# Optimization experiments

Measured on AMD Instinct MI355X. Metric: run time of the kernel, lower is better.

## Reference

```python
import jax, jax.numpy as jnp
import numpy as np
import math

B, S, DM, H = 2, 2048, 1024, 16
HD = DM // H  # head_dim = 64


def setup_inputs() -> dict:
    key = jax.random.key(0)
    ks = jax.random.split(key, 7)
    mk = lambda k, shp, s=1.0: jax.random.normal(k, shp, dtype=jnp.float32) * s
    return {
        "q": mk(ks[0], (B, S, DM)),
        "k": mk(ks[1], (B, S, DM)),
        "v": mk(ks[2], (B, S, DM)),
        "wq": mk(ks[3], (DM, DM), 0.02),
        "wk": mk(ks[4], (DM, DM), 0.02),
        "wv": mk(ks[5], (DM, DM), 0.02),
        "wo": mk(ks[6], (DM, DM), 0.02),
    }


def reference(q, k, v, wq, wk, wv, wo):
    bsz, seqlen, _ = q.shape
    # bias-free linear projections: y = x @ W.T (torch nn.Linear layout [out,in])
    def proj(x, w):
        y = jnp.einsum('bsd,ed->bse', x, w)
        return y.reshape(bsz, seqlen, H, HD).transpose(0, 2, 1, 3)  # (B,H,S,HD)
    xq, xk, xv = proj(q, wq), proj(k, wk), proj(v, wv)
    scores = jnp.einsum('bhqd,bhkd->bhqk', xq, xk) / math.sqrt(HD)  # (B,H,S,S)
    # causal mask: -inf above the diagonal
    causal = jnp.tril(jnp.ones((seqlen, seqlen), dtype=bool))
    scores = jnp.where(causal[None, None], scores, -jnp.inf)
    probs = jax.nn.softmax(scores.astype(jnp.float32), axis=-1).astype(xq.dtype)
    # dropout p=0.0 -> identity in eval / p=0 config
    out = jnp.einsum('bhqk,bhkd->bhqd', probs, xv)  # (B,H,S,HD)
    out = out.transpose(0, 2, 1, 3).reshape(bsz, seqlen, DM)
    return jnp.einsum('bsd,ed->bse', out, wo)
```

## Files before the change

### kernel.cpp

```cpp
#include <hip/hip_runtime.h>
#include <hip/hip_bf16.h>
#include <stdint.h>

#define NB 2
#define NS 2048
#define NDM 1024
#define NH 16
#define NHD 64
#define NTOK (NB * NS)

typedef __bf16 bf16x8 __attribute__((ext_vector_type(8)));
typedef float f32x4 __attribute__((ext_vector_type(4)));
typedef uint16_t u16x8 __attribute__((ext_vector_type(8)));

static __device__ __forceinline__ uint16_t f2bf(float f) {
  __bf16 b = (__bf16)f;
  union { __bf16 b; uint16_t u; } x; x.b = b;
  return x.u;
}

static __device__ __forceinline__ u16x8 cvt8(float4 a, float4 b) {
  u16x8 v;
  v[0] = f2bf(a.x); v[1] = f2bf(a.y); v[2] = f2bf(a.z); v[3] = f2bf(a.w);
  v[4] = f2bf(b.x); v[5] = f2bf(b.y); v[6] = f2bf(b.z); v[7] = f2bf(b.w);
  return v;
}

static __device__ __forceinline__ void gload_lds16(const void* g, void* l) {
  __builtin_amdgcn_global_load_lds(
      (const __attribute__((address_space(1))) void*)g,
      (__attribute__((address_space(3))) void*)l, 16, 0, 0);
}

__global__ __launch_bounds__(256) void cvt_w(
    const float* __restrict__ w0, const float* __restrict__ w1,
    const float* __restrict__ w2, const float* __restrict__ w3,
    uint16_t* __restrict__ o0, uint16_t* __restrict__ o1,
    uint16_t* __restrict__ o2, uint16_t* __restrict__ o3) {
  int y = blockIdx.y;
  const float* src = (y == 0) ? w0 : (y == 1) ? w1 : (y == 2) ? w2 : w3;
  uint16_t* dst = (y == 0) ? o0 : (y == 1) ? o1 : (y == 2) ? o2 : o3;
  int i = ((int)blockIdx.x * 256 + (int)threadIdx.x) * 8;
  float4 a = *(const float4*)(src + i);
  float4 b = *(const float4*)(src + i + 4);
  *(u16x8*)&dst[i] = cvt8(a, b);
}

__global__ __launch_bounds__(256) void proj_gemm(
    const float* __restrict__ q, const float* __restrict__ k,
    const float* __restrict__ v, const uint16_t* __restrict__ wqb,
    const uint16_t* __restrict__ wkb, const uint16_t* __restrict__ wvb,
    uint16_t* __restrict__ XQ, uint16_t* __restrict__ XK,
    uint16_t* __restrict__ XVT) {
  __shared__ uint16_t As[2][128][64];
  __shared__ uint16_t Bs[2][128][64];
  int z = blockIdx.z;
  const float* A = (z == 0) ? q : (z == 1) ? k : v;
  const uint16_t* W = (z == 0) ? wqb : (z == 1) ? wkb : wvb;
  int m0 = blockIdx.x * 128, n0 = blockIdx.y * 128;
  int tid = threadIdx.x;
  int lane = tid & 63, w = tid >> 6;
  int g = lane >> 4, r16 = lane & 15;
  int wm = w >> 1, wn = w & 1;
  int bce = ((lane & 7) ^ ((lane >> 3) & 7)) * 8;
  int brlane = lane >> 3;

  f32x4 acc[4][4] = {};
  float4 a0[4], a1[4];

  #pragma unroll
  for (int cc = 0; cc < 4; ++cc) {
    int ch = tid + cc * 256;
    int row = ch >> 3, c8 = ch & 7;
    const float* src = A + (size_t)(m0 + row) * NDM + c8 * 8;
    a0[cc] = *(const float4*)src;
    a1[cc] = *(const float4*)(src + 4);
  }
  #pragma unroll
  for (int i = 0; i < 4; ++i) {
    int brow = w * 32 + i * 8;
    gload_lds16(W + (size_t)(n0 + brow + brlane) * NDM + bce, &Bs[0][brow][0]);
  }
  #pragma unroll
  for (int cc = 0; cc < 4; ++cc) {
    int ch = tid + cc * 256;
    int row = ch >> 3, c8 = ch & 7;
    *(u16x8*)&As[0][row][((c8 ^ (row & 7)) * 8)] = cvt8(a0[cc], a1[cc]);
  }
  #pragma unroll
  for (int cc = 0; cc < 4; ++cc) {
    int ch = tid + cc * 256;
    int row = ch >> 3, c8 = ch & 7;
    const float* src = A + (size_t)(m0 + row) * NDM + 64 + c8 * 8;
    a0[cc] = *(const float4*)src;
    a1[cc] = *(const float4*)(src + 4);
  }
  __syncthreads();

  for (int t = 0; t < 16; ++t) {
    int cur = t & 1, nxt = cur ^ 1;
    if (t < 15) {
      int k1 = (t + 1) * 64;
      #pragma unroll
      for (int i = 0; i < 4; ++i) {
        int brow = w * 32 + i * 8;
        gload_lds16(W + (size_t)(n0 + brow + brlane) * NDM + k1 + bce,
                    &Bs[nxt][brow][0]);
      }
      #pragma unroll
      for (int cc = 0; cc < 4; ++cc) {
        int ch = tid + cc * 256;
        int row = ch >> 3, c8 = ch & 7;
        *(u16x8*)&As[nxt][row][((c8 ^ (row & 7)) * 8)] = cvt8(a0[cc], a1[cc]);
      }
      if (t < 14) {
        int k2 = (t + 2) * 64;
        #pragma unroll
        for (int cc = 0; cc < 4; ++cc) {
          int ch = tid + cc * 256;
          int row = ch >> 3, c8 = ch & 7;
          const float* src = A + (size_t)(m0 + row) * NDM + k2 + c8 * 8;
          a0[cc] = *(const float4*)src;
          a1[cc] = *(const float4*)(src + 4);
        }
      }
    }

    #pragma unroll
    for (int kc = 0; kc < 2; ++kc) {
      bf16x8 af[4], bf[4];
      #pragma unroll
      for (int i = 0; i < 4; ++i) {
        int gran = (kc * 4 + g) ^ (r16 & 7);
        af[i] = *(const bf16x8*)&As[cur][wm * 64 + i * 16 + r16][gran * 8];
        bf[i] = *(const bf16x8*)&Bs[cur][wn * 64 + i * 16 + r16][gran * 8];
      }
      #pragma unroll
      for (int mi = 0; mi < 4; ++mi)
        #pragma unroll
        for (int ni = 0; ni < 4; ++ni)
          acc[mi][ni] = __builtin_amdgcn_mfma_f32_16x16x32_bf16(
              af[mi], bf[ni], acc[mi][ni], 0, 0, 0);
    }
    __syncthreads();
  }

  float scale = (z == 0) ? 0.125f * 1.44269504088896340736f : 1.0f;
  #pragma unroll
  for (int mi = 0; mi < 4; ++mi) {
    #pragma unroll
    for (int ni = 0; ni < 4; ++ni) {
      int m = m0 + wm * 64 + mi * 16 + g * 4;
      int n = n0 + wn * 64 + ni * 16 + r16;
      f32x4 a = acc[mi][ni];
      if (z == 2) {
        ushort4 pk;
        pk.x = f2bf(a[0]); pk.y = f2bf(a[1]);
        pk.z = f2bf(a[2]); pk.w = f2bf(a[3]);
        *(ushort4*)&XVT[(size_t)n * NTOK + m] = pk;
      } else {
        uint16_t* Y = (z == 0) ? XQ : XK;
        #pragma unroll
        for (int j = 0; j < 4; ++j)
          Y[(size_t)(m + j) * NDM + n] = f2bf(a[j] * scale);
      }
    }
  }
}

__global__ __launch_bounds__(256) void attn_kernel(
    const uint16_t* __restrict__ XQ, const uint16_t* __restrict__ XK,
    const uint16_t* __restrict__ XVT, uint16_t* __restrict__ AO) {
  __shared__ uint16_t Klds[64][72];
  __shared__ uint16_t Vlds[64][72];
  __shared__ uint16_t Plds[4][16][72];

  int tid = threadIdx.x;
  int lane = tid & 63;
  int w = tid >> 6;
  int g = lane >> 4, r16 = lane & 15;
  int srow = tid >> 2;
  int scol = (tid & 3) * 16;

  int item = (int)blockIdx.x;
  int qc = 31 - (item >> 5);
  int bh = item & 31;
  int b = bh >> 4, h = bh & 15;
  int q0 = qc * 64;
  int q0w = q0 + w * 16;
  int T = qc + 1;

  const uint16_t* qb =
      XQ + (size_t)(b * NS + q0w + r16) * NDM + h * NHD + g * 8;
  bf16x8 qf0 = *(const bf16x8*)qb;
  bf16x8 qf1 = *(const bf16x8*)(qb + 32);

  f32x4 oacc[4] = {};
  float mrow = -1e30f, lsum = 0.f;

  const uint16_t* kbase = XK + (size_t)(b * NS + srow) * NDM + h * NHD + scol;
  const uint16_t* vbase = XVT + (size_t)(h * NHD + srow) * NTOK + b * NS + scol;

  u16x8 kr0 = *(const u16x8*)(kbase);
  u16x8 kr1 = *(const u16x8*)(kbase + 8);
  u16x8 vr0 = *(const u16x8*)(vbase);
  u16x8 vr1 = *(const u16x8*)(vbase + 8);

  for (int t = 0; t < T; ++t) {
    int kv0 = t * 64;
    __syncthreads();
    *(u16x8*)&Klds[srow][scol]     = kr0;
    *(u16x8*)&Klds[srow][scol + 8] = kr1;
    *(u16x8*)&Vlds[srow][scol]     = vr0;
    *(u16x8*)&Vlds[srow][scol + 8] = vr1;
    __syncthreads();
    if (t + 1 < T) {
      const uint16_t* kp = kbase + (size_t)(t + 1) * 64 * NDM;
      const uint16_t* vp = vbase + (t + 1) * 64;
      kr0 = *(const u16x8*)(kp);
      kr1 = *(const u16x8*)(kp + 8);
      vr0 = *(const u16x8*)(vp);
      vr1 = *(const u16x8*)(vp + 8);
    }

    f32x4 sc[4];
    __builtin_amdgcn_s_setprio(1);
    #pragma unroll
    for (int t4 = 0; t4 < 4; ++t4) {
      bf16x8 kf0 = *(const bf16x8*)&Klds[t4 * 16 + r16][g * 8];
      bf16x8 kf1 = *(const bf16x8*)&Klds[t4 * 16 + r16][32 + g * 8];
      f32x4 x = __builtin_amdgcn_mfma_f32_16x16x32_bf16(
          kf0, qf0, (f32x4){0.f, 0.f, 0.f, 0.f}, 0, 0, 0);
      x = __builtin_amdgcn_mfma_f32_16x16x32_bf16(kf1, qf1, x, 0, 0, 0);
      sc[t4] = x;
    }
    __builtin_amdgcn_s_setprio(0);

    #pragma unroll
    for (int t4 = 0; t4 < 4; ++t4) {
      if (kv0 + t4 * 16 + 15 > q0w) {
        #pragma unroll
        for (int j = 0; j < 4; ++j)
          if (kv0 + t4 * 16 + g * 4 + j > q0w + r16) sc[t4][j] = -1e30f;
      }
    }

    float m16 = fmaxf(
        fmaxf(fmaxf(fmaxf(sc[0][0], sc[0][1]), fmaxf(sc[0][2], sc[0][3])),
              fmaxf(fmaxf(sc[1][0], sc[1][1]), fmaxf(sc[1][2], sc[1][3]))),
        fmaxf(fmaxf(fmaxf(sc[2][0], sc[2][1]), fmaxf(sc[2][2], sc[2][3])),
              fmaxf(fmaxf(sc[3][0], sc[3][1]), fmaxf(sc[3][2], sc[3][3]))));
    m16 = fmaxf(m16, __shfl_xor(m16, 16));
    m16 = fmaxf(m16, __shfl_xor(m16, 32));

    if (!__all(m16 <= mrow + 8.0f)) {
      float mnew = fmaxf(mrow, m16);
      float sf = __builtin_amdgcn_exp2f(mrow - mnew);
      mrow = mnew;
      lsum *= sf;
      #pragma unroll
      for (int j = 0; j < 4; ++j) {
        float sfj = __shfl(sf, g * 4 + j);
        #pragma unroll
        for (int dt = 0; dt < 4; ++dt) oacc[dt][j] *= sfj;
      }
    }

    #pragma unroll
    for (int t4 = 0; t4 < 4; ++t4) {
      float p0 = __builtin_amdgcn_exp2f(sc[t4][0] - mrow);
      float p1 = __builtin_amdgcn_exp2f(sc[t4][1] - mrow);
      float p2 = __builtin_amdgcn_exp2f(sc[t4][2] - mrow);
      float p3 = __builtin_amdgcn_exp2f(sc[t4][3] - mrow);
      lsum += (p0 + p1) + (p2 + p3);
      ushort4 pk;
      pk.x = f2bf(p0); pk.y = f2bf(p1); pk.z = f2bf(p2); pk.w = f2bf(p3);
      *(ushort4*)&Plds[w][r16][t4 * 16 + g * 4] = pk;
    }

    bf16x8 pa0 = *(const bf16x8*)&Plds[w][r16][g * 8];
    bf16x8 pa1 = *(const bf16x8*)&Plds[w][r16][32 + g * 8];
    __builtin_amdgcn_s_setprio(1);
    #pragma unroll
    for (int dt = 0; dt < 4; ++dt) {
      bf16x8 vf0 = *(const bf16x8*)&Vlds[dt * 16 + r16][g * 8];
      bf16x8 vf1 = *(const bf16x8*)&Vlds[dt * 16 + r16][32 + g * 8];
      oacc[dt] = __builtin_amdgcn_mfma_f32_16x16x32_bf16(pa0, vf0, oacc[dt], 0, 0, 0);
      oacc[dt] = __builtin_amdgcn_mfma_f32_16x16x32_bf16(pa1, vf1, oacc[dt], 0, 0, 0);
    }
    __builtin_amdgcn_s_setprio(0);
  }

  float l2 = lsum + __shfl_xor(lsum, 16);
  float ltot = l2 + __shfl_xor(l2, 32);
  #pragma unroll
  for (int j = 0; j < 4; ++j) {
    float lt = __shfl(ltot, g * 4 + j);
    float inv = 1.0f / lt;
    size_t ro = (size_t)(b * NS + q0 + w * 16 + g * 4 + j) * NDM + h * NHD;
    #pragma unroll
    for (int dt = 0; dt < 4; ++dt)
      AO[ro + dt * 16 + r16] = f2bf(oacc[dt][j] * inv);
  }
}

__global__ __launch_bounds__(256) void out_gemm(
    const uint16_t* __restrict__ AO, const uint16_t* __restrict__ wob,
    float* __restrict__ out) {
  __shared__ uint16_t As[2][128][64];
  __shared__ uint16_t Bs[2][128][64];
  int m0 = blockIdx.x * 128, n0 = blockIdx.y * 128;
  int tid = threadIdx.x;
  int lane = tid & 63, w = tid >> 6;
  int g = lane >> 4, r16 = lane & 15;
  int wm = w >> 1, wn = w & 1;
  int bce = ((lane & 7) ^ ((lane >> 3) & 7)) * 8;
  int brlane = lane >> 3;

  f32x4 acc[4][4] = {};

  #pragma unroll
  for (int i = 0; i < 4; ++i) {
    int row = w * 32 + i * 8;
    gload_lds16(AO + (size_t)(m0 + row + brlane) * NDM + bce, &As[0][row][0]);
    gload_lds16(wob + (size_t)(n0 + row + brlane) * NDM + bce, &Bs[0][row][0]);
  }
  __syncthreads();

  for (int t = 0; t < 16; ++t) {
    int cur = t & 1, nxt = cur ^ 1;
    if (t < 15) {
      int k1 = (t + 1) * 64;
      #pragma unroll
      for (int i = 0; i < 4; ++i) {
        int row = w * 32 + i * 8;
        gload_lds16(AO + (size_t)(m0 + row + brlane) * NDM + k1 + bce,
                    &As[nxt][row][0]);
        gload_lds16(wob + (size_t)(n0 + row + brlane) * NDM + k1 + bce,
                    &Bs[nxt][row][0]);
      }
    }

    #pragma unroll
    for (int kc = 0; kc < 2; ++kc) {
      bf16x8 af[4], bf[4];
      #pragma unroll
      for (int i = 0; i < 4; ++i) {
        int gran = (kc * 4 + g) ^ (r16 & 7);
        af[i] = *(const bf16x8*)&As[cur][wm * 64 + i * 16 + r16][gran * 8];
        bf[i] = *(const bf16x8*)&Bs[cur][wn * 64 + i * 16 + r16][gran * 8];
      }
      #pragma unroll
      for (int mi = 0; mi < 4; ++mi)
        #pragma unroll
        for (int ni = 0; ni < 4; ++ni)
          acc[mi][ni] = __builtin_amdgcn_mfma_f32_16x16x32_bf16(
              af[mi], bf[ni], acc[mi][ni], 0, 0, 0);
    }
    __syncthreads();
  }

  #pragma unroll
  for (int mi = 0; mi < 4; ++mi) {
    #pragma unroll
    for (int ni = 0; ni < 4; ++ni) {
      int m = m0 + wm * 64 + mi * 16 + g * 4;
      int n = n0 + wn * 64 + ni * 16 + r16;
      #pragma unroll
      for (int j = 0; j < 4; ++j)
        out[(size_t)(m + j) * NDM + n] = acc[mi][ni][j];
    }
  }
}

extern "C" void kernel_launch(void* const* d_in, const int* in_sizes, int n_in,
                              void* d_out, int out_size, void* d_ws,
                              size_t ws_size, hipStream_t stream) {
  const float* q  = (const float*)d_in[0];
  const float* k  = (const float*)d_in[1];
  const float* v  = (const float*)d_in[2];
  const float* wq = (const float*)d_in[3];
  const float* wk = (const float*)d_in[4];
  const float* wv = (const float*)d_in[5];
  const float* wo = (const float*)d_in[6];

  uint16_t* XQ  = (uint16_t*)d_ws;
  uint16_t* XK  = XQ + (size_t)NTOK * NDM;
  uint16_t* XVT = XK + (size_t)NTOK * NDM;
  uint16_t* AO  = XVT + (size_t)NTOK * NDM;
  uint16_t* WQB = AO + (size_t)NTOK * NDM;
  uint16_t* WKB = WQB + (size_t)NDM * NDM;
  uint16_t* WVB = WKB + (size_t)NDM * NDM;
  uint16_t* WOB = WVB + (size_t)NDM * NDM;

  cvt_w<<<dim3(NDM * NDM / (256 * 8), 4), 256, 0, stream>>>(
      wq, wk, wv, wo, WQB, WKB, WVB, WOB);
  proj_gemm<<<dim3(NTOK / 128, NDM / 128, 3), 256, 0, stream>>>(
      q, k, v, WQB, WKB, WVB, XQ, XK, XVT);
  attn_kernel<<<dim3(1024), 256, 0, stream>>>(XQ, XK, XVT, AO);
  out_gemm<<<dim3(NTOK / 128, NDM / 128), 256, 0, stream>>>(
      AO, WOB, (float*)d_out);
}
```

Measured before the change: 120.1 us.

## Load GEMM A operand and attention K/V fragments directly from global memory

The projection GEMM no longer stages the fp32 activation tile through shared memory. Each wave loads its own A fragments straight from global memory at MFMA time and converts them to bf16 in registers. The attention kernel drops its K/V shared-memory tiles and block barriers, reading fragments directly from global memory per wave, and lets a wave skip KV tiles that lie fully above its causal diagonal. This removes LDS traffic and syncs, at the cost of redundant, less coalesced global loads with no software prefetch, so the loop is exposed to memory latency.

```diff
diff --git a/kernel.cpp b/kernel.cpp
--- a/kernel.cpp
+++ b/kernel.cpp
@@ -24,6 +24,12 @@
   v[0] = f2bf(a.x); v[1] = f2bf(a.y); v[2] = f2bf(a.z); v[3] = f2bf(a.w);
   v[4] = f2bf(b.x); v[5] = f2bf(b.y); v[6] = f2bf(b.z); v[7] = f2bf(b.w);
   return v;
+}
+
+static __device__ __forceinline__ bf16x8 cvt8f(float4 a, float4 b) {
+  union { u16x8 u; bf16x8 h; } r;
+  r.u = cvt8(a, b);
+  return r.h;
 }
 
 static __device__ __forceinline__ void gload_lds16(const void* g, void* l) {
@@ -52,7 +58,6 @@
     const uint16_t* __restrict__ wkb, const uint16_t* __restrict__ wvb,
     uint16_t* __restrict__ XQ, uint16_t* __restrict__ XK,
     uint16_t* __restrict__ XVT) {
-  __shared__ uint16_t As[2][128][64];
   __shared__ uint16_t Bs[2][128][64];
   int z = blockIdx.z;
   const float* A = (z == 0) ? q : (z == 1) ? k : v;
@@ -66,63 +71,27 @@
   int brlane = lane >> 3;
 
   f32x4 acc[4][4] = {};
-  float4 a0[4], a1[4];
-
-  #pragma unroll
-  for (int cc = 0; cc < 4; ++cc) {
-    int ch = tid + cc * 256;
-    int row = ch >> 3, c8 = ch & 7;
-    const float* src = A + (size_t)(m0 + row) * NDM + c8 * 8;
-    a0[cc] = *(const float4*)src;
-    a1[cc] = *(const float4*)(src + 4);
-  }
+
   #pragma unroll
   for (int i = 0; i < 4; ++i) {
     int brow = w * 32 + i * 8;
     gload_lds16(W + (size_t)(n0 + brow + brlane) * NDM + bce, &Bs[0][brow][0]);
   }
-  #pragma unroll
-  for (int cc = 0; cc < 4; ++cc) {
-    int ch = tid + cc * 256;
-    int row = ch >> 3, c8 = ch & 7;
-    *(u16x8*)&As[0][row][((c8 ^ (row & 7)) * 8)] = cvt8(a0[cc], a1[cc]);
-  }
-  #pragma unroll
-  for (int cc = 0; cc < 4; ++cc) {
-    int ch = tid + cc * 256;
-    int row = ch >> 3, c8 = ch & 7;
-    const float* src = A + (size_t)(m0 + row) * NDM + 64 + c8 * 8;
-    a0[cc] = *(const float4*)src;
-    a1[cc] = *(const float4*)(src + 4);
-  }
   __syncthreads();
+
+  const float* arow[4];
+  #pragma unroll
+  for (int i = 0; i < 4; ++i)
+    arow[i] = A + (size_t)(m0 + wm * 64 + i * 16 + r16) * NDM + g * 8;
 
   for (int t = 0; t < 16; ++t) {
     int cur = t & 1, nxt = cur ^ 1;
     if (t < 15) {
-      int k1 = (t + 1) * 64;
       #pragma unroll
       for (int i = 0; i < 4; ++i) {
         int brow = w * 32 + i * 8;
-        gload_lds16(W + (size_t)(n0 + brow + brlane) * NDM + k1 + bce,
+        gload_lds16(W + (size_t)(n0 + brow + brlane) * NDM + (t + 1) * 64 + bce,
                     &Bs[nxt][brow][0]);
-      }
-      #pragma unroll
-      for (int cc = 0; cc < 4; ++cc) {
-        int ch = tid + cc * 256;
-        int row = ch >> 3, c8 = ch & 7;
-        *(u16x8*)&As[nxt][row][((c8 ^ (row & 7)) * 8)] = cvt8(a0[cc], a1[cc]);
-      }
-      if (t < 14) {
-        int k2 = (t + 2) * 64;
-        #pragma unroll
-        for (int cc = 0; cc < 4; ++cc) {
-          int ch = tid + cc * 256;
-          int row = ch >> 3, c8 = ch & 7;
-          const float* src = A + (size_t)(m0 + row) * NDM + k2 + c8 * 8;
-          a0[cc] = *(const float4*)src;
-          a1[cc] = *(const float4*)(src + 4);
-        }
       }
     }
 
@@ -131,8 +100,14 @@
       bf16x8 af[4], bf[4];
       #pragma unroll
       for (int i = 0; i < 4; ++i) {
+        const float* ap = arow[i] + t * 64 + kc * 32;
+        float4 f0 = *(const float4*)ap;
+        float4 f1 = *(const float4*)(ap + 4);
+        af[i] = cvt8f(f0, f1);
+      }
+      #pragma unroll
+      for (int i = 0; i < 4; ++i) {
         int gran = (kc * 4 + g) ^ (r16 & 7);
-        af[i] = *(const bf16x8*)&As[cur][wm * 64 + i * 16 + r16][gran * 8];
         bf[i] = *(const bf16x8*)&Bs[cur][wn * 64 + i * 16 + r16][gran * 8];
       }
       #pragma unroll
@@ -171,16 +146,12 @@
 __global__ __launch_bounds__(256) void attn_kernel(
     const uint16_t* __restrict__ XQ, const uint16_t* __restrict__ XK,
     const uint16_t* __restrict__ XVT, uint16_t* __restrict__ AO) {
-  __shared__ uint16_t Klds[64][72];
-  __shared__ uint16_t Vlds[64][72];
   __shared__ uint16_t Plds[4][16][72];
 
   int tid = threadIdx.x;
   int lane = tid & 63;
   int w = tid >> 6;
   int g = lane >> 4, r16 = lane & 15;
-  int srow = tid >> 2;
-  int scol = (tid & 3) * 16;
 
   int item = (int)blockIdx.x;
   int qc = 31 - (item >> 5);
@@ -198,37 +169,20 @@
   f32x4 oacc[4] = {};
   float mrow = -1e30f, lsum = 0.f;
 
-  const uint16_t* kbase = XK + (size_t)(b * NS + srow) * NDM + h * NHD + scol;
-  const uint16_t* vbase = XVT + (size_t)(h * NHD + srow) * NTOK + b * NS + scol;
-
-  u16x8 kr0 = *(const u16x8*)(kbase);
-  u16x8 kr1 = *(const u16x8*)(kbase + 8);
-  u16x8 vr0 = *(const u16x8*)(vbase);
-  u16x8 vr1 = *(const u16x8*)(vbase + 8);
+  const uint16_t* kfb = XK + (size_t)(b * NS) * NDM + h * NHD;
+  const uint16_t* vfb = XVT + (size_t)(h * NHD) * NTOK + b * NS;
 
   for (int t = 0; t < T; ++t) {
     int kv0 = t * 64;
-    __syncthreads();
-    *(u16x8*)&Klds[srow][scol]     = kr0;
-    *(u16x8*)&Klds[srow][scol + 8] = kr1;
-    *(u16x8*)&Vlds[srow][scol]     = vr0;
-    *(u16x8*)&Vlds[srow][scol + 8] = vr1;
-    __syncthreads();
-    if (t + 1 < T) {
-      const uint16_t* kp = kbase + (size_t)(t + 1) * 64 * NDM;
-      const uint16_t* vp = vbase + (t + 1) * 64;
-      kr0 = *(const u16x8*)(kp);
-      kr1 = *(const u16x8*)(kp + 8);
-      vr0 = *(const u16x8*)(vp);
-      vr1 = *(const u16x8*)(vp + 8);
-    }
+    if (kv0 > q0w + 15) continue;
 
     f32x4 sc[4];
     __builtin_amdgcn_s_setprio(1);
     #pragma unroll
     for (int t4 = 0; t4 < 4; ++t4) {
-      bf16x8 kf0 = *(const bf16x8*)&Klds[t4 * 16 + r16][g * 8];
-      bf16x8 kf1 = *(const bf16x8*)&Klds[t4 * 16 + r16][32 + g * 8];
+      const uint16_t* kr = kfb + (size_t)(kv0 + t4 * 16 + r16) * NDM + g * 8;
+      bf16x8 kf0 = *(const bf16x8*)kr;
+      bf16x8 kf1 = *(const bf16x8*)(kr + 32);
       f32x4 x = __builtin_amdgcn_mfma_f32_16x16x32_bf16(
           kf0, qf0, (f32x4){0.f, 0.f, 0.f, 0.f}, 0, 0, 0);
       x = __builtin_amdgcn_mfma_f32_16x16x32_bf16(kf1, qf1, x, 0, 0, 0);
@@ -283,8 +237,9 @@
     __builtin_amdgcn_s_setprio(1);
     #pragma unroll
     for (int dt = 0; dt < 4; ++dt) {
-      bf16x8 vf0 = *(const bf16x8*)&Vlds[dt * 16 + r16][g * 8];
-      bf16x8 vf1 = *(const bf16x8*)&Vlds[dt * 16 + r16][32 + g * 8];
+      const uint16_t* vr = vfb + (size_t)(dt * 16 + r16) * NTOK + kv0 + g * 8;
+      bf16x8 vf0 = *(const bf16x8*)vr;
+      bf16x8 vf1 = *(const bf16x8*)(vr + 32);
       oacc[dt] = __builtin_amdgcn_mfma_f32_16x16x32_bf16(pa0, vf0, oacc[dt], 0, 0, 0);
       oacc[dt] = __builtin_amdgcn_mfma_f32_16x16x32_bf16(pa1, vf1, oacc[dt], 0, 0, 0);
     }
```

Measured after the change: 286.7 us. 2.39x slower.
